# Performance work log

Hardware: AMD Instinct MI355X
Metric: run time of the kernel (lower is better)

## Reference

```python
import jax, jax.numpy as jnp
import numpy as np

L, H, NH, NKV, HD, I, V, B, S = 18, 640, 4, 1, 256, 2048, 32768, 1, 1024
WINDOW = 512
EPS = 1e-6
THETA_G = 1000000.0
THETA_L = 10000.0


def _rms(x, w):
    # Gemma RMSNorm: x / rms(x) * (1 + w)
    var = jnp.mean(jnp.square(x), axis=-1, keepdims=True)
    return x * jax.lax.rsqrt(var + EPS) * (1.0 + w)


def _rope_tables(theta):
    inv = 1.0 / (theta ** (jnp.arange(0, HD, 2, dtype=jnp.float32) / HD))
    f = jnp.arange(S, dtype=jnp.float32)[:, None] * inv[None, :]
    emb = jnp.concatenate([f, f], axis=-1)  # [S, HD]
    return jnp.cos(emb), jnp.sin(emb)


def _rope(x, cos, sin):
    # x: [B, S, n, HD]
    x1, x2 = jnp.split(x, 2, axis=-1)
    rot = jnp.concatenate([-x2, x1], axis=-1)
    return x * cos[None, :, None, :] + rot * sin[None, :, None, :]


def setup_inputs() -> dict:
    key = jax.random.key(0)
    ks = jax.random.split(key, 16)
    r = lambda k, sh: jax.random.normal(k, sh, jnp.float32) * 0.02
    return {
        'input_ids': jax.random.randint(ks[0], (B, S), 0, V, jnp.int32),
        'is_full': jnp.array([(i + 1) % 6 == 0 for i in range(L)]),
        'embed': r(ks[1], (V, H)),
        'wq': r(ks[2], (L, H, NH * HD)),
        'wk': r(ks[3], (L, H, NKV * HD)),
        'wv': r(ks[4], (L, H, NKV * HD)),
        'wo': r(ks[5], (L, NH * HD, H)),
        'qn': jnp.zeros((L, HD)), 'kn': jnp.zeros((L, HD)),
        'ln1': jnp.zeros((L, H)), 'ln2': jnp.zeros((L, H)),
        'ln3': jnp.zeros((L, H)), 'ln4': jnp.zeros((L, H)),
        'wg': r(ks[6], (L, H, I)), 'wu': r(ks[7], (L, H, I)),
        'wd': r(ks[8], (L, I, H)),
        'norm_w': jnp.zeros((H,)),
    }


def _forward(embed, wq, wk, wv, wo, qn, kn, ln1, ln2, ln3, ln4, wg, wu, wd,
             norm_w, input_ids, is_full):
    cos_g, sin_g = _rope_tables(THETA_G)
    cos_l, sin_l = _rope_tables(THETA_L)
    pos = jnp.arange(S)
    causal = pos[:, None] >= pos[None, :]
    sliding = causal & ((pos[:, None] - pos[None, :]) < WINDOW)
    scale = HD ** -0.5
    grp = NH // NKV

    h = embed[input_ids] * jnp.asarray(H ** 0.5, embed.dtype)  # [B,S,H]

    def body(h, xs):
        (wq_, wk_, wv_, wo_, qn_, kn_, l1, l2, l3, l4, wg_, wu_, wd_, full) = xs
        cos = jnp.where(full, cos_g, cos_l)
        sin = jnp.where(full, sin_g, sin_l)
        mask = jnp.where(full, causal, sliding)
        x = _rms(h, l1)
        q = (x @ wq_).reshape(B, S, NH, HD)
        k = (x @ wk_).reshape(B, S, NKV, HD)
        v = (x @ wv_).reshape(B, S, NKV, HD)
        q = _rope(_rms(q, qn_), cos, sin)
        k = _rope(_rms(k, kn_), cos, sin)
        qg = q.reshape(B, S, NKV, grp, HD)
        scores = jnp.einsum('bqngd,bsnd->bngqs', qg, k) * scale
        scores = jnp.where(mask[None, None, None], scores, -1e30)
        attn = jax.nn.softmax(scores, axis=-1)
        o = jnp.einsum('bngqs,bsnd->bqngd', attn, v).reshape(B, S, NH * HD)
        h = h + _rms(o @ wo_, l2)               # post_attention_layernorm then residual
        x = _rms(h, l3)                          # pre_feedforward_layernorm
        mlp = (jax.nn.gelu(x @ wg_, approximate=True) * (x @ wu_)) @ wd_  # GeGLU
        h = h + _rms(mlp, l4)                    # post_feedforward_layernorm then residual
        return h, None

    h, _ = jax.lax.scan(body, h, (wq, wk, wv, wo, qn, kn, ln1, ln2, ln3, ln4, wg, wu, wd, is_full))
    h = _rms(h, norm_w)
    # lm_head tied to embed_tokens; final_logit_softcapping = 0.0 (disabled)
    return jnp.einsum('bsh,vh->bsv', h, embed)


def reference(input_ids, is_full, embed, wq, wk, wv, wo, qn, kn,
              ln1, ln2, ln3, ln4, wg, wu, wd, norm_w):
    return _forward(embed, wq, wk, wv, wo, qn, kn, ln1, ln2, ln3, ln4,
                    wg, wu, wd, norm_w, input_ids, is_full)
```

## Files before the change

### kernel.cpp

```cpp
#include <hip/hip_runtime.h>


typedef unsigned short u16;
typedef __attribute__((ext_vector_type(4))) float f32x4;
typedef __attribute__((ext_vector_type(8))) short bf16x8;

#define DEV static __device__ __forceinline__
#define BIGN (1 << 30)

DEV u16 f2bf(float f) {
  union { float f; unsigned u; } x; x.f = f;
  unsigned r = x.u + 0x7fffu + ((x.u >> 16) & 1u);
  return (u16)(r >> 16);
}

#define GLOAD16(gp, lp) __builtin_amdgcn_global_load_lds( \
    (const __attribute__((address_space(1))) void*)(gp), \
    (__attribute__((address_space(3))) void*)(lp), 16, 0, 0)

DEV float blockSum(float v, float* red) {
#pragma unroll
  for (int o = 32; o; o >>= 1) v += __shfl_down(v, o);
  int lane = threadIdx.x & 63, wid = threadIdx.x >> 6;
  if (lane == 0) red[wid] = v;
  __syncthreads();
  float s = red[0] + red[1] + red[2] + red[3];
  __syncthreads();
  return s;
}

DEV float blockMax(float v, float* red) {
#pragma unroll
  for (int o = 32; o; o >>= 1) v = fmaxf(v, __shfl_down(v, o));
  int lane = threadIdx.x & 63, wid = threadIdx.x >> 6;
  if (lane == 0) red[wid] = v;
  __syncthreads();
  float s = fmaxf(fmaxf(red[0], red[1]), fmaxf(red[2], red[3]));
  __syncthreads();
  return s;
}

DEV void cstore(float* C, size_t i, float v) { C[i] = v; }
DEV void cstore(u16* C, size_t i, float v) { C[i] = f2bf(v); }

template <typename CT, int GEGLU, int BMODE>
__global__ __launch_bounds__(256) void gemm_nt(
    const u16* __restrict__ A, int lda, long sA,
    const void* __restrict__ B0v, int ldb0,
    const void* __restrict__ B1v, int ldb1,
    const void* __restrict__ B2v, int ldb2,
    int ns1, int ns2,
    CT* __restrict__ C, int ldc, long sC,
    int K, float alpha, int kmode, int nshift, int ksplit) {
  __shared__ __align__(16) u16 As[2 * 128 * 64];
  __shared__ __align__(16) u16 Bs[2 * 128 * 64];
  int m0, n0;
  if (nshift == -3) {
    int b = blockIdx.x;
    m0 = ((b >> 3) & 7) * 128;
    n0 = ((b >> 6) * 8 + (b & 7)) * 128;
  } else {
    m0 = blockIdx.y * 128;
    if (nshift == -1) n0 = blockIdx.x * 128;
    else if (nshift == -2) { n0 = blockIdx.x * 128; if (n0 > m0) return; }
    else { n0 = m0 - nshift + blockIdx.x * 128; if (n0 < 0) return; }
  }
  int klo = 0, khi = K;
  if (kmode == 1) { klo = m0 - 512; if (klo < 0) klo = 0; khi = m0 + 128; if (khi > K) khi = K; }
  else if (kmode == 2) { khi = m0 + 128; if (khi > K) khi = K; }
  else if (kmode == 3) { int kl = K / ksplit; klo = blockIdx.z * kl; khi = klo + kl; }
  A += (long)blockIdx.z * sA;

  const int t = threadIdx.x;
  const int l = t & 63, w = t >> 6;
  const int wr = w >> 1, wc = w & 1;
  const int lr = l & 15, lk = l >> 4;
  const int axr = lr & 7;
  const int srow = t >> 3;
  const int scolx = ((t & 7) ^ (srow & 7)) << 3;
  const u16* Ag = A + (size_t)(m0 + srow) * lda + scolx;
  const int nsteps = (khi - klo) >> 6;

  auto stageA = [&](int db, int k0) {
    u16* al = As + db * 8192 + w * 512;
#pragma unroll
    for (int p = 0; p < 4; ++p)
      GLOAD16(Ag + k0 + (size_t)(32 * p) * lda, al + p * 2048);
  };

  const u16* Bg16 = nullptr;
  const float* Bp = nullptr; int bldb = 0, bcol = 0, krow0 = 0;
  f32x4 fb[8];
  if constexpr (BMODE == 0) {
    Bg16 = (const u16*)B0v + (size_t)(n0 + srow) * ldb0 + scolx;
  } else {
    int rv = n0 + (l & 31) * 4;
    if (GEGLU) {
      int half = (rv >> 4) & 1;
      Bp = (const float*)(half ? B1v : B0v);
      bldb = half ? ldb1 : ldb0;
      bcol = (rv >> 5) * 16 + (rv & 15);
    } else if (rv >= ns2) { Bp = (const float*)B2v; bldb = ldb2; bcol = rv - ns2; }
    else if (rv >= ns1)   { Bp = (const float*)B1v; bldb = ldb1; bcol = rv - ns1; }
    else                  { Bp = (const float*)B0v; bldb = ldb0; bcol = rv; }
    krow0 = w * 16 + (l >> 5) * 8;
  }

  auto stageB0 = [&](int db, int k0) {
    u16* bl = Bs + db * 8192 + w * 512;
#pragma unroll
    for (int p = 0; p < 4; ++p)
      GLOAD16(Bg16 + k0 + (size_t)(32 * p) * ldb0, bl + p * 2048);
  };
  auto loadB = [&](int k0) {
#pragma unroll
    for (int j = 0; j < 8; ++j)
      fb[j] = *(const f32x4*)&Bp[(size_t)(k0 + krow0 + j) * bldb + bcol];
  };
  auto writeB = [&](int db) {
    int kb = w * 2 + (l >> 5);
#pragma unroll
    for (int e = 0; e < 4; ++e) {
      int row = (l & 31) * 4 + e;
      u16 tmp[8];
#pragma unroll
      for (int j = 0; j < 8; ++j) tmp[j] = f2bf(fb[j][e]);
      *(int4*)&Bs[db * 8192 + row * 64 + ((kb ^ (row & 7)) << 3)] = *(int4*)tmp;
    }
  };

  f32x4 acc[4][4] = {};
  auto compute = [&](int db) {
    const u16* Ab = As + db * 8192;
    const u16* Bb = Bs + db * 8192;
    bf16x8 af[2][4], bfr[2][4];
#pragma unroll
    for (int kk = 0; kk < 2; ++kk)
#pragma unroll
      for (int i = 0; i < 4; ++i) {
        af[kk][i]  = *(const bf16x8*)&Ab[(wr * 64 + i * 16 + lr) * 64 + (((kk * 4 + lk) ^ axr) << 3)];
        bfr[kk][i] = *(const bf16x8*)&Bb[(wc * 64 + i * 16 + lr) * 64 + (((kk * 4 + lk) ^ axr) << 3)];
      }
#pragma unroll
    for (int kk = 0; kk < 2; ++kk)
#pragma unroll
      for (int mi = 0; mi < 4; ++mi)
#pragma unroll
        for (int ni = 0; ni < 4; ++ni)
          acc[mi][ni] = __builtin_amdgcn_mfma_f32_16x16x32_bf16(af[kk][mi], bfr[kk][ni], acc[mi][ni], 0, 0, 0);
  };

  if constexpr (BMODE == 0) {
    stageA(0, klo); stageB0(0, klo);
    for (int s = 0; s < nsteps; ++s) {
      __syncthreads();
      const int db = s & 1;
      if (s + 1 < nsteps) { stageA(db ^ 1, klo + (s + 1) * 64); stageB0(db ^ 1, klo + (s + 1) * 64); }
      compute(db);
    }
  } else {
    loadB(klo); stageA(0, klo);
    for (int s = 0; s < nsteps; ++s) {
      const int db = s & 1;
      writeB(db);
      if (s + 1 < nsteps) loadB(klo + (s + 1) * 64);
      __syncthreads();
      if (s + 1 < nsteps) stageA(db ^ 1, klo + (s + 1) * 64);
      compute(db);
    }
  }

  C += (long)blockIdx.z * sC;
  if (GEGLU) {
#pragma unroll
    for (int mi = 0; mi < 4; ++mi) {
      int row = m0 + wr * 64 + mi * 16 + lk * 4;
#pragma unroll
      for (int np = 0; np < 2; ++np) {
        int col = (n0 + wc * 64) / 2 + np * 16 + lr;
#pragma unroll
        for (int j = 0; j < 4; ++j) {
          float g = acc[mi][2 * np][j], u = acc[mi][2 * np + 1][j];
          float z = 0.7978845608028654f * (g + 0.044715f * g * g * g);
          float th = 2.0f / (1.0f + __expf(-2.0f * z)) - 1.0f;
          cstore(C, (size_t)(row + j) * ldc + col, 0.5f * g * (1.0f + th) * u);
        }
      }
    }
  } else {
#pragma unroll
    for (int mi = 0; mi < 4; ++mi) {
      int row = m0 + wr * 64 + mi * 16 + lk * 4;
#pragma unroll
      for (int ni = 0; ni < 4; ++ni) {
        int col = n0 + wc * 64 + ni * 16 + lr;
#pragma unroll
        for (int j = 0; j < 4; ++j)
          cstore(C, (size_t)(row + j) * ldc + col, acc[mi][ni][j] * alpha);
      }
    }
  }
}

__global__ void conv_bf16_kernel(const float* __restrict__ in, u16* __restrict__ out, long n4) {
  for (long i = (long)blockIdx.x * blockDim.x + threadIdx.x; i < n4; i += (long)gridDim.x * blockDim.x) {
    float4 v = ((const float4*)in)[i];
    ushort4 o4 = { f2bf(v.x), f2bf(v.y), f2bf(v.z), f2bf(v.w) };
    ((ushort4*)out)[i] = o4;
  }
}

__global__ void gather_rms_kernel(const int* __restrict__ ids, const float* __restrict__ embed,
                                  const float* __restrict__ w, float* __restrict__ h,
                                  u16* __restrict__ x) {
  __shared__ float red[8];
  const int s = blockIdx.x, t = threadIdx.x;
  const float* src = embed + (size_t)ids[s] * 640;
  const float scale = sqrtf(640.0f);
  float hv[3];
  float ss = 0.0f;
#pragma unroll
  for (int i = 0; i < 3; ++i) {
    int c = t + i * 256;
    float v = (c < 640) ? src[c] * scale : 0.0f;
    hv[i] = v; ss += v * v;
  }
  ss = blockSum(ss, red);
  const float sc = rsqrtf(ss * (1.0f / 640.0f) + 1e-6f);
#pragma unroll
  for (int i = 0; i < 3; ++i) {
    int c = t + i * 256;
    if (c < 640) {
      h[(size_t)s * 640 + c] = hv[i];
      x[(size_t)s * 640 + c] = f2bf(hv[i] * sc * (1.0f + w[c]));
    }
  }
}

__global__ void fused_add_norm(float* __restrict__ h, const float* __restrict__ t1,
                               int nsl, const float* __restrict__ wa,
                               const float* __restrict__ wn, u16* __restrict__ xout) {
  __shared__ float red[8];
  const int row = blockIdx.x, t = threadIdx.x;
  float ts[3], hv[3];
  float ss = 0.0f;
#pragma unroll
  for (int i = 0; i < 3; ++i) {
    int c = t + i * 256;
    float v = 0.0f;
    if (c < 640) {
      v = t1[(size_t)row * 640 + c];
      for (int z = 1; z < nsl; ++z) v += t1[(size_t)z * 655360 + (size_t)row * 640 + c];
    }
    ts[i] = v; ss += v * v;
  }
  ss = blockSum(ss, red);
  const float s1 = rsqrtf(ss * (1.0f / 640.0f) + 1e-6f);
  float ss2 = 0.0f;
#pragma unroll
  for (int i = 0; i < 3; ++i) {
    int c = t + i * 256;
    float v = 0.0f;
    if (c < 640) v = h[(size_t)row * 640 + c] + ts[i] * s1 * (1.0f + wa[c]);
    hv[i] = v; ss2 += v * v;
  }
  ss2 = blockSum(ss2, red);
  const float s2 = rsqrtf(ss2 * (1.0f / 640.0f) + 1e-6f);
#pragma unroll
  for (int i = 0; i < 3; ++i) {
    int c = t + i * 256;
    if (c < 640) {
      h[(size_t)row * 640 + c] = hv[i];
      xout[(size_t)row * 640 + c] = f2bf(hv[i] * s2 * (1.0f + wn[c]));
    }
  }
}

__global__ void rope_tables_kernel(float* cg, float* sg, float* cl, float* sl) {
  int s = blockIdx.x, t = threadIdx.x;
  float e = -(float)t * (1.0f / 128.0f);
  float ag = (float)s * expf(e * logf(1000000.0f));
  float al = (float)s * expf(e * logf(10000.0f));
  cg[s * 128 + t] = cosf(ag); sg[s * 128 + t] = sinf(ag);
  cl[s * 128 + t] = cosf(al); sl[s * 128 + t] = sinf(al);
}

__global__ void rope_fused(const float* __restrict__ qkvf, const float* __restrict__ qn,
                           const float* __restrict__ kn, u16* __restrict__ qb,
                           u16* __restrict__ kb,
                           const float* __restrict__ ct, const float* __restrict__ st) {
  __shared__ float red[8];
  __shared__ float sh[256];
  const int s = blockIdx.x, hh = blockIdx.y, t = threadIdx.x;
  const float* src = qkvf + (size_t)s * 1536 + hh * 256;
  const float* nw = (hh == 4) ? kn : qn;
  float x = src[t];
  float ss = blockSum(x * x, red);
  float n = x * rsqrtf(ss * (1.0f / 256.0f) + 1e-6f) * (1.0f + nw[t]);
  sh[t] = n;
  __syncthreads();
  float cosv = ct[s * 128 + (t & 127)];
  float sinv = st[s * 128 + (t & 127)];
  float partner = (t < 128) ? -sh[t + 128] : sh[t - 128];
  u16 r = f2bf(n * cosv + partner * sinv);
  if (hh == 4) kb[(size_t)s * 256 + t] = r;
  else qb[((size_t)hh * 1024 + s) * 256 + t] = r;
}

__global__ void softmax_kernel(const float* __restrict__ sc, u16* __restrict__ P, int mode) {
  __shared__ float red[8];
  const int i = blockIdx.x, hh = blockIdx.y, t = threadIdx.x;
  const float* row = sc + ((size_t)hh * 1024 + i) * 1024;
  u16* prow = P + ((size_t)hh * 1024 + i) * 1024;
  const int m0 = i & ~127;
  int lo = 0, wlo = 0;
  if (mode) {
    lo = i - 511; if (lo < 0) lo = 0;
    wlo = m0 - 512; if (wlo < 0) wlo = 0;
  }
  const int whi = m0 + 127;
  float m = -1e30f;
  for (int j = lo + t; j <= i; j += 256) m = fmaxf(m, row[j]);
  m = blockMax(m, red);
  float sum = 0.0f;
  for (int j = lo + t; j <= i; j += 256) sum += __expf(row[j] - m);
  sum = blockSum(sum, red);
  float inv = 1.0f / sum;
  for (int j = wlo + t; j <= whi; j += 256) {
    float v = (j >= lo && j <= i) ? __expf(row[j] - m) * inv : 0.0f;
    prow[j] = f2bf(v);
  }
}

extern "C" void kernel_launch(void* const* d_in, const int* in_sizes, int n_in,
                              void* d_out, int out_size, void* d_ws, size_t ws_size,
                              hipStream_t stream) {
  (void)in_sizes; (void)n_in; (void)out_size; (void)ws_size;
  const int*   ids   = (const int*)d_in[0];
  const float* embed = (const float*)d_in[2];
  const float* wq    = (const float*)d_in[3];
  const float* wk    = (const float*)d_in[4];
  const float* wv    = (const float*)d_in[5];
  const float* wo    = (const float*)d_in[6];
  const float* qn    = (const float*)d_in[7];
  const float* kn    = (const float*)d_in[8];
  const float* ln1   = (const float*)d_in[9];
  const float* ln2   = (const float*)d_in[10];
  const float* ln3   = (const float*)d_in[11];
  const float* ln4   = (const float*)d_in[12];
  const float* wg    = (const float*)d_in[13];
  const float* wu    = (const float*)d_in[14];
  const float* wd    = (const float*)d_in[15];
  const float* nw    = (const float*)d_in[16];
  float* out = (float*)d_out;

  const int S = 1024, H = 640, NH = 4, HD = 256, I = 2048, V = 32768;

  unsigned char* p = (unsigned char*)d_ws;
  auto alloc = [&](size_t b) { void* r = (void*)p; p += (b + 255) & ~(size_t)255; return r; };
  u16*   embT  = (u16*)alloc((size_t)V * H * 2);
  float* h     = (float*)alloc((size_t)S * H * 4);
  u16*   x     = (u16*)alloc((size_t)S * H * 2);
  float* qkvf  = (float*)alloc((size_t)S * 1536 * 4);
  u16*   qb    = (u16*)alloc((size_t)NH * S * HD * 2);
  u16*   kb    = (u16*)alloc((size_t)S * HD * 2);
  float* scp   = (float*)alloc((size_t)NH * S * S * 4);
  u16*   P     = (u16*)alloc((size_t)NH * S * S * 2);
  u16*   o     = (u16*)alloc((size_t)S * NH * HD * 2);
  float* t1    = (float*)alloc((size_t)4 * S * H * 4);
  u16*   mg    = (u16*)alloc((size_t)S * I * 2);
  u16*   hn    = (u16*)alloc((size_t)S * H * 2);
  float* cg    = (float*)alloc((size_t)S * 128 * 4);
  float* sg    = (float*)alloc((size_t)S * 128 * 4);
  float* cl    = (float*)alloc((size_t)S * 128 * 4);
  float* sl2   = (float*)alloc((size_t)S * 128 * 4);

  rope_tables_kernel<<<S, 128, 0, stream>>>(cg, sg, cl, sl2);
  conv_bf16_kernel<<<2048, 256, 0, stream>>>(embed, embT, (long)V * H / 4);
  gather_rms_kernel<<<S, 256, 0, stream>>>(ids, embed, ln1, h, x);

  for (int l = 0; l < 18; ++l) {
    bool full = ((l + 1) % 6) == 0;
    const float* wq_l = wq + (size_t)l * H * 1024;
    const float* wk_l = wk + (size_t)l * H * 256;
    const float* wv_l = wv + (size_t)l * H * 256;
    const float* wo_l = wo + (size_t)l * 1024 * H;
    const float* wg_l = wg + (size_t)l * H * I;
    const float* wu_l = wu + (size_t)l * H * I;
    const float* wd_l = wd + (size_t)l * I * H;

    gemm_nt<float, 0, 1><<<dim3(12, 8, 1), 256, 0, stream>>>(
        x, H, 0, wq_l, 1024, wk_l, 256, wv_l, 256, 1024, 1280,
        qkvf, 1536, 0, H, 1.0f, 0, -1, 1);
    rope_fused<<<dim3(S, 5), 256, 0, stream>>>(qkvf, qn + l * HD, kn + l * HD, qb, kb,
                                               full ? cg : cl, full ? sg : sl2);
    if (full)
      gemm_nt<float, 0, 0><<<dim3(8, 8, NH), 256, 0, stream>>>(
          qb, HD, (long)S * HD, kb, HD, nullptr, 0, nullptr, 0, BIGN, BIGN,
          scp, S, (long)S * S, HD, 0.0625f, 0, -2, 1);
    else
      gemm_nt<float, 0, 0><<<dim3(5, 8, NH), 256, 0, stream>>>(
          qb, HD, (long)S * HD, kb, HD, nullptr, 0, nullptr, 0, BIGN, BIGN,
          scp, S, (long)S * S, HD, 0.0625f, 0, 512, 1);
    softmax_kernel<<<dim3(S, NH), 256, 0, stream>>>(scp, P, full ? 0 : 1);
    gemm_nt<u16, 0, 1><<<dim3(2, 8, NH), 256, 0, stream>>>(
        P, S, (long)S * S, qkvf + 1280, 1536, nullptr, 0, nullptr, 0, BIGN, BIGN,
        o, NH * HD, HD, S, 1.0f, full ? 2 : 1, -1, 1);
    gemm_nt<float, 0, 1><<<dim3(5, 8, 2), 256, 0, stream>>>(
        o, NH * HD, 0, wo_l, 640, nullptr, 0, nullptr, 0, BIGN, BIGN,
        t1, H, (long)S * H, NH * HD, 1.0f, 3, -1, 2);
    fused_add_norm<<<S, 256, 0, stream>>>(h, t1, 2, ln2 + l * H, ln3 + l * H, x);

    gemm_nt<u16, 1, 1><<<dim3(32, 8, 1), 256, 0, stream>>>(
        x, H, 0, wg_l, 2048, wu_l, 2048, nullptr, 0, BIGN, BIGN,
        mg, I, 0, H, 1.0f, 0, -1, 1);
    gemm_nt<float, 0, 1><<<dim3(5, 8, 4), 256, 0, stream>>>(
        mg, I, 0, wd_l, 640, nullptr, 0, nullptr, 0, BIGN, BIGN,
        t1, H, (long)S * H, I, 1.0f, 3, -1, 4);
    fused_add_norm<<<S, 256, 0, stream>>>(h, t1, 4, ln4 + l * H,
                                          (l == 17) ? nw : ln1 + (l + 1) * H,
                                          (l == 17) ? hn : x);
  }

  gemm_nt<float, 0, 0><<<dim3(2048, 1, 1), 256, 0, stream>>>(
      hn, H, 0, embT, H, nullptr, 0, nullptr, 0, BIGN, BIGN,
      out, V, 0, H, 1.0f, 0, -3, 1);
}
```

Measured before the change: 2.380 ms.

## Replace QK/softmax/PV kernel chain with fused flash attention kernel

Replaces the separate scores GEMM, softmax kernel and PV GEMM with a single flash-attention kernel that does online softmax in registers, computing QK^T via MFMA, masking causally or by sliding window, and accumulating P·V. This removes the round trips of the fp32 score matrix and the bf16 probability matrix through global memory. The QKV projection now uses split-K of two, and the rope kernel sums the two partials and also writes a transposed bf16 V. The fused kernel launches only 64 blocks with launch_bounds(256,1), so GPU occupancy is low, and each block walks all of its key tiles serially.

```diff
diff --git a/kernel.cpp b/kernel.cpp
--- a/kernel.cpp
+++ b/kernel.cpp
@@ -25,17 +25,6 @@
   if (lane == 0) red[wid] = v;
   __syncthreads();
   float s = red[0] + red[1] + red[2] + red[3];
-  __syncthreads();
-  return s;
-}
-
-DEV float blockMax(float v, float* red) {
-#pragma unroll
-  for (int o = 32; o; o >>= 1) v = fmaxf(v, __shfl_down(v, o));
-  int lane = threadIdx.x & 63, wid = threadIdx.x >> 6;
-  if (lane == 0) red[wid] = v;
-  __syncthreads();
-  float s = fmaxf(fmaxf(red[0], red[1]), fmaxf(red[2], red[3]));
   __syncthreads();
   return s;
 }
@@ -202,6 +191,136 @@
   }
 }
 
+__global__ __launch_bounds__(256, 1) void flash_attn(
+    const u16* __restrict__ qb, const u16* __restrict__ kb,
+    const u16* __restrict__ vt, u16* __restrict__ o, int isfull) {
+  __shared__ __align__(16) u16 Ks[4 * 64 * 64];
+  __shared__ __align__(16) u16 Vs[256 * 64];
+  __shared__ __align__(16) u16 Ps[4][16][80];
+  const int m0 = blockIdx.x * 64, z = blockIdx.y;
+  const int t = threadIdx.x;
+  const int l = t & 63, w = t >> 6;
+  const int lr = l & 15, lk = l >> 4;
+  const int srow = t >> 3;
+  const int scolx = ((t & 7) ^ (srow & 7)) << 3;
+
+  bf16x8 afq[8];
+  {
+    const u16* qp = qb + (size_t)(z * 1024 + m0 + w * 16 + lr) * 256 + lk * 8;
+#pragma unroll
+    for (int kk = 0; kk < 8; ++kk) afq[kk] = *(const bf16x8*)(qp + kk * 32);
+  }
+
+  const int klo = isfull ? 0 : (m0 - 512 > 0 ? m0 - 512 : 0);
+  const int ntiles = (m0 + 64 - klo) >> 6;
+  const int qrow_base = m0 + w * 16 + (l >> 4) * 4;
+
+  float m_run[4] = {-1e30f, -1e30f, -1e30f, -1e30f};
+  float l_run[4] = {};
+  f32x4 oacc[16] = {};
+
+  for (int tile = 0; tile < ntiles; ++tile) {
+    const int k0 = klo + tile * 64;
+    __syncthreads();
+#pragma unroll
+    for (int c = 0; c < 4; ++c)
+#pragma unroll
+      for (int p = 0; p < 2; ++p)
+        GLOAD16(kb + (size_t)(k0 + srow + 32 * p) * 256 + c * 64 + scolx,
+                Ks + c * 4096 + p * 2048 + w * 512);
+#pragma unroll
+    for (int p = 0; p < 8; ++p)
+      GLOAD16(vt + (size_t)(srow + 32 * p) * 1024 + k0 + scolx,
+              Vs + p * 2048 + w * 512);
+    __syncthreads();
+
+    f32x4 sacc[4] = {};
+#pragma unroll
+    for (int kk = 0; kk < 8; ++kk) {
+      bf16x8 bfr[4];
+#pragma unroll
+      for (int ni = 0; ni < 4; ++ni) {
+        int row = ni * 16 + lr;
+        bfr[ni] = *(const bf16x8*)&Ks[(kk >> 1) * 4096 + row * 64 +
+                                      ((((kk & 1) * 4 + lk) ^ (row & 7)) << 3)];
+      }
+#pragma unroll
+      for (int ni = 0; ni < 4; ++ni)
+        sacc[ni] = __builtin_amdgcn_mfma_f32_16x16x32_bf16(afq[kk], bfr[ni], sacc[ni], 0, 0, 0);
+    }
+
+    float sv[4][4], mx[4], rs[4], sf[4];
+#pragma unroll
+    for (int j = 0; j < 4; ++j) mx[j] = -1e30f;
+#pragma unroll
+    for (int ni = 0; ni < 4; ++ni)
+#pragma unroll
+      for (int j = 0; j < 4; ++j) {
+        int q = qrow_base + j, s = k0 + ni * 16 + lr;
+        bool valid = (s <= q) && (isfull || s >= q - 511);
+        float v = valid ? sacc[ni][j] * 0.0625f : -1e30f;
+        sv[ni][j] = v;
+        mx[j] = fmaxf(mx[j], v);
+      }
+#pragma unroll
+    for (int j = 0; j < 4; ++j) {
+#pragma unroll
+      for (int d = 1; d < 16; d <<= 1) mx[j] = fmaxf(mx[j], __shfl_xor(mx[j], d));
+      float mn = fmaxf(m_run[j], mx[j]);
+      sf[j] = __expf(m_run[j] - mn);
+      m_run[j] = mn;
+      rs[j] = 0.0f;
+    }
+    float pv[4][4];
+#pragma unroll
+    for (int ni = 0; ni < 4; ++ni)
+#pragma unroll
+      for (int j = 0; j < 4; ++j) {
+        float p = (sv[ni][j] <= -1e29f) ? 0.0f : __expf(sv[ni][j] - m_run[j]);
+        pv[ni][j] = p;
+        rs[j] += p;
+      }
+#pragma unroll
+    for (int j = 0; j < 4; ++j) {
+#pragma unroll
+      for (int d = 1; d < 16; d <<= 1) rs[j] += __shfl_xor(rs[j], d);
+      l_run[j] = l_run[j] * sf[j] + rs[j];
+    }
+#pragma unroll
+    for (int nd = 0; nd < 16; ++nd)
+#pragma unroll
+      for (int j = 0; j < 4; ++j) oacc[nd][j] *= sf[j];
+
+#pragma unroll
+    for (int ni = 0; ni < 4; ++ni)
+#pragma unroll
+      for (int j = 0; j < 4; ++j)
+        Ps[w][(l >> 4) * 4 + j][ni * 16 + (l & 15)] = f2bf(pv[ni][j]);
+    bf16x8 ap[2];
+#pragma unroll
+    for (int kk = 0; kk < 2; ++kk)
+      ap[kk] = *(const bf16x8*)&Ps[w][lr][kk * 32 + lk * 8];
+
+#pragma unroll
+    for (int nd = 0; nd < 16; ++nd)
+#pragma unroll
+      for (int kk = 0; kk < 2; ++kk) {
+        int row = nd * 16 + lr;
+        bf16x8 bv = *(const bf16x8*)&Vs[row * 64 + (((kk * 4 + lk) ^ (row & 7)) << 3)];
+        oacc[nd] = __builtin_amdgcn_mfma_f32_16x16x32_bf16(ap[kk], bv, oacc[nd], 0, 0, 0);
+      }
+  }
+
+#pragma unroll
+  for (int nd = 0; nd < 16; ++nd)
+#pragma unroll
+    for (int j = 0; j < 4; ++j) {
+      int q = qrow_base + j;
+      int d = z * 256 + nd * 16 + (l & 15);
+      o[(size_t)q * 1024 + d] = f2bf(oacc[nd][j] / l_run[j]);
+    }
+}
+
 __global__ void conv_bf16_kernel(const float* __restrict__ in, u16* __restrict__ out, long n4) {
   for (long i = (long)blockIdx.x * blockDim.x + threadIdx.x; i < n4; i += (long)gridDim.x * blockDim.x) {
     float4 v = ((const float4*)in)[i];
@@ -287,14 +406,20 @@
 
 __global__ void rope_fused(const float* __restrict__ qkvf, const float* __restrict__ qn,
                            const float* __restrict__ kn, u16* __restrict__ qb,
-                           u16* __restrict__ kb,
+                           u16* __restrict__ kb, u16* __restrict__ vt,
                            const float* __restrict__ ct, const float* __restrict__ st) {
   __shared__ float red[8];
   __shared__ float sh[256];
   const int s = blockIdx.x, hh = blockIdx.y, t = threadIdx.x;
-  const float* src = qkvf + (size_t)s * 1536 + hh * 256;
+  const long SL = (long)1024 * 1536;
+  if (hh == 5) {
+    long i = (size_t)s * 1536 + 1280 + t;
+    vt[(size_t)t * 1024 + s] = f2bf(qkvf[i] + qkvf[i + SL]);
+    return;
+  }
+  long i = (size_t)s * 1536 + hh * 256 + t;
   const float* nw = (hh == 4) ? kn : qn;
-  float x = src[t];
+  float x = qkvf[i] + qkvf[i + SL];
   float ss = blockSum(x * x, red);
   float n = x * rsqrtf(ss * (1.0f / 256.0f) + 1e-6f) * (1.0f + nw[t]);
   sh[t] = n;
@@ -305,31 +430,6 @@
   u16 r = f2bf(n * cosv + partner * sinv);
   if (hh == 4) kb[(size_t)s * 256 + t] = r;
   else qb[((size_t)hh * 1024 + s) * 256 + t] = r;
-}
-
-__global__ void softmax_kernel(const float* __restrict__ sc, u16* __restrict__ P, int mode) {
-  __shared__ float red[8];
-  const int i = blockIdx.x, hh = blockIdx.y, t = threadIdx.x;
-  const float* row = sc + ((size_t)hh * 1024 + i) * 1024;
-  u16* prow = P + ((size_t)hh * 1024 + i) * 1024;
-  const int m0 = i & ~127;
-  int lo = 0, wlo = 0;
-  if (mode) {
-    lo = i - 511; if (lo < 0) lo = 0;
-    wlo = m0 - 512; if (wlo < 0) wlo = 0;
-  }
-  const int whi = m0 + 127;
-  float m = -1e30f;
-  for (int j = lo + t; j <= i; j += 256) m = fmaxf(m, row[j]);
-  m = blockMax(m, red);
-  float sum = 0.0f;
-  for (int j = lo + t; j <= i; j += 256) sum += __expf(row[j] - m);
-  sum = blockSum(sum, red);
-  float inv = 1.0f / sum;
-  for (int j = wlo + t; j <= whi; j += 256) {
-    float v = (j >= lo && j <= i) ? __expf(row[j] - m) * inv : 0.0f;
-    prow[j] = f2bf(v);
-  }
 }
 
 extern "C" void kernel_launch(void* const* d_in, const int* in_sizes, int n_in,
@@ -361,11 +461,10 @@
   u16*   embT  = (u16*)alloc((size_t)V * H * 2);
   float* h     = (float*)alloc((size_t)S * H * 4);
   u16*   x     = (u16*)alloc((size_t)S * H * 2);
-  float* qkvf  = (float*)alloc((size_t)S * 1536 * 4);
+  float* qkvf  = (float*)alloc((size_t)2 * S * 1536 * 4);
   u16*   qb    = (u16*)alloc((size_t)NH * S * HD * 2);
   u16*   kb    = (u16*)alloc((size_t)S * HD * 2);
-  float* scp   = (float*)alloc((size_t)NH * S * S * 4);
-  u16*   P     = (u16*)alloc((size_t)NH * S * S * 2);
+  u16*   vt    = (u16*)alloc((size_t)HD * S * 2);
   u16*   o     = (u16*)alloc((size_t)S * NH * HD * 2);
   float* t1    = (float*)alloc((size_t)4 * S * H * 4);
   u16*   mg    = (u16*)alloc((size_t)S * I * 2);
@@ -389,23 +488,12 @@
     const float* wu_l = wu + (size_t)l * H * I;
     const float* wd_l = wd + (size_t)l * I * H;
 
-    gemm_nt<float, 0, 1><<<dim3(12, 8, 1), 256, 0, stream>>>(
+    gemm_nt<float, 0, 1><<<dim3(12, 8, 2), 256, 0, stream>>>(
         x, H, 0, wq_l, 1024, wk_l, 256, wv_l, 256, 1024, 1280,
-        qkvf, 1536, 0, H, 1.0f, 0, -1, 1);
-    rope_fused<<<dim3(S, 5), 256, 0, stream>>>(qkvf, qn + l * HD, kn + l * HD, qb, kb,
+        qkvf, 1536, (long)S * 1536, H, 1.0f, 3, -1, 2);
+    rope_fused<<<dim3(S, 6), 256, 0, stream>>>(qkvf, qn + l * HD, kn + l * HD, qb, kb, vt,
                                                full ? cg : cl, full ? sg : sl2);
-    if (full)
-      gemm_nt<float, 0, 0><<<dim3(8, 8, NH), 256, 0, stream>>>(
-          qb, HD, (long)S * HD, kb, HD, nullptr, 0, nullptr, 0, BIGN, BIGN,
-          scp, S, (long)S * S, HD, 0.0625f, 0, -2, 1);
-    else
-      gemm_nt<float, 0, 0><<<dim3(5, 8, NH), 256, 0, stream>>>(
-          qb, HD, (long)S * HD, kb, HD, nullptr, 0, nullptr, 0, BIGN, BIGN,
-          scp, S, (long)S * S, HD, 0.0625f, 0, 512, 1);
-    softmax_kernel<<<dim3(S, NH), 256, 0, stream>>>(scp, P, full ? 0 : 1);
-    gemm_nt<u16, 0, 1><<<dim3(2, 8, NH), 256, 0, stream>>>(
-        P, S, (long)S * S, qkvf + 1280, 1536, nullptr, 0, nullptr, 0, BIGN, BIGN,
-        o, NH * HD, HD, S, 1.0f, full ? 2 : 1, -1, 1);
+    flash_attn<<<dim3(16, NH), 256, 0, stream>>>(qb, kb, vt, o, full ? 1 : 0);
     gemm_nt<float, 0, 1><<<dim3(5, 8, 2), 256, 0, stream>>>(
         o, NH * HD, 0, wo_l, 640, nullptr, 0, nullptr, 0, BIGN, BIGN,
         t1, H, (long)S * H, NH * HD, 1.0f, 3, -1, 2);
```

After: 2.385 ms. About the same (+0.2%).
